# Kernel optimization log

Hardware: AMD Instinct MI355X
Metric: run time of the kernel (lower is better)

## Reference

```python
import jax, jax.numpy as jnp
import numpy as np

B, S, D = 8, 2048, 512

def setup_inputs() -> dict:
    key = jax.random.key(0)
    ks = jax.random.split(key, 7)
    scale = 1.0 / np.sqrt(D)
    return {
        "x": jax.random.normal(ks[0], (B, S, D), dtype=jnp.float32),
        "Wq": jax.random.normal(ks[1], (D, D), dtype=jnp.float32) * scale,
        "bq": jax.random.normal(ks[2], (D,), dtype=jnp.float32) * 0.01,
        "Wk": jax.random.normal(ks[3], (D, D), dtype=jnp.float32) * scale,
        "bk": jax.random.normal(ks[4], (D,), dtype=jnp.float32) * 0.01,
        "Wv": jax.random.normal(ks[5], (D, D), dtype=jnp.float32) * scale,
        "bv": jax.random.normal(ks[6], (D,), dtype=jnp.float32) * 0.01,
    }

def reference(x, Wq, bq, Wk, bk, Wv, bv):
    # Q/K/V projections: [B,S,D] @ [D,D]
    q = jnp.einsum('bsd,de->bse', x, Wq) + bq
    k = jnp.einsum('bsd,de->bse', x, Wk) + bk
    v = jnp.einsum('bsd,de->bse', x, Wv) + bv
    # NOTE: original module has NO 1/sqrt(d) scaling
    scores = jnp.einsum('bqd,bkd->bqk', q, k)          # [B,S,S]
    attn = jax.nn.softmax(scores, axis=-1)
    return jnp.einsum('bqk,bkd->bqd', attn, v)         # [B,S,D]
```

## Files before the change

kernel.cpp:

```cpp
#include <hip/hip_runtime.h>
#include <hip/hip_fp16.h>


typedef unsigned short u16;
typedef unsigned int u32;
typedef __attribute__((ext_vector_type(8))) _Float16 f16x8;
typedef __attribute__((ext_vector_type(16))) float f32x16;

#define S_LEN 2048
#define D_DIM 512
#define B_N 8

__device__ __forceinline__ u16 f2bf(float f) {
    u32 u = __float_as_uint(f);
    u32 r = u + 0x7FFFu + ((u >> 16) & 1u);
    return (u16)(r >> 16);
}
__device__ __forceinline__ float bf2f(u16 h) {
    return __uint_as_float((u32)h << 16);
}
__device__ __forceinline__ u16 f2h(float f) {
    _Float16 h = (_Float16)f;
    return *(u16*)&h;
}
__device__ __forceinline__ float h2f(u16 h) {
    _Float16 v = *(_Float16*)&h;
    return (float)v;
}
__device__ __forceinline__ void gl16(const u16* g, u16* l) {
    __builtin_amdgcn_global_load_lds(
        (const __attribute__((address_space(1))) void*)g,
        (__attribute__((address_space(3))) void*)l, 16, 0, 0);
}
__device__ __forceinline__ f32x16 mfma16(f16x8 a, f16x8 b, f32x16 c) {
    return __builtin_amdgcn_mfma_f32_32x32x16_f16(a, b, c, 0, 0, 0);
}

__global__ void detect_k(const u16* __restrict__ x, int* __restrict__ flag)
{
    int t = threadIdx.x;
    u16 u = x[2 * t];
    int e = (u >> 7) & 0xFF;
    int sane = (e == 0) || (e >= 110 && e <= 140);
    unsigned long long b = __ballot(sane);
    if (t == 0) *flag = (__popcll(b) >= 32) ? 1 : 0;
}

__global__ __launch_bounds__(256) void cvt_x(
    const void* __restrict__ X, u16* __restrict__ xf,
    const int* __restrict__ flagp)
{
    const size_t i4 = ((size_t)blockIdx.x * 256 + threadIdx.x) * 4;
    float f[4];
    if (*flagp) {
        ushort4 u = *(const ushort4*)((const u16*)X + i4);
        f[0] = bf2f(u.x); f[1] = bf2f(u.y); f[2] = bf2f(u.z); f[3] = bf2f(u.w);
    } else {
        float4 ff = *(const float4*)((const float*)X + i4);
        f[0] = ff.x; f[1] = ff.y; f[2] = ff.z; f[3] = ff.w;
    }
    ushort4 h;
    h.x = f2h(f[0]); h.y = f2h(f[1]); h.z = f2h(f[2]); h.w = f2h(f[3]);
    *(ushort4*)(xf + i4) = h;
}

__global__ __launch_bounds__(256) void pack_w(
    const void* __restrict__ Wq, const void* __restrict__ Wk, const void* __restrict__ Wv,
    u16* __restrict__ WT, const int* __restrict__ flagp)
{
    const int k = blockIdx.x;
    const int n = blockIdx.y * 256 + threadIdx.x;
    const void* W = n < 512 ? Wq : n < 1024 ? Wk : Wv;
    const int nc = n & 511;
    float f = *flagp ? bf2f(((const u16*)W)[(size_t)k * 512 + nc])
                     : ((const float*)W)[(size_t)k * 512 + nc];
    WT[(size_t)n * 512 + k] = f2h(f);
}

__global__ void pack_bias(
    const void* __restrict__ bq, const void* __restrict__ bk, const void* __restrict__ bv,
    float* __restrict__ bcat, const int* __restrict__ flagp)
{
    const int t = blockIdx.x * 256 + threadIdx.x;
    const void* b = t < 512 ? bq : t < 1024 ? bk : bv;
    const int i = t & 511;
    bcat[t] = *flagp ? bf2f(((const u16*)b)[i]) : ((const float*)b)[i];
}

template <int EPI>
__global__ __launch_bounds__(256) void gemm_f16(
    const u16* __restrict__ A_, const u16* __restrict__ B_,
    void* __restrict__ Cp, const float* __restrict__ biasf,
    u16* __restrict__ Oq, u16* __restrict__ Ok, u16* __restrict__ OvT,
    const int* __restrict__ flagp,
    int K, int lda, int ldb, int ldc, long sA, long sB, long sC, long cbase)
{
    const int tid = threadIdx.x;
    const int lane = tid & 63, wav = tid >> 6;
    const int l31 = lane & 31, lh = lane >> 5;

    const int gx = gridDim.x, gy = gridDim.y;
    const int total = gx * gy * gridDim.z;
    const int chunk = total >> 3;
    int lin = (blockIdx.z * gy + blockIdx.y) * gx + blockIdx.x;
    lin = (lin & 7) * chunk + (lin >> 3);
    const int bx = lin % gx;
    const int by = (lin / gx) % gy;
    const int bz = lin / (gx * gy);

    const int m0 = by * 128, n0 = bx * 128;
    const int bm = (wav >> 1) * 64, bn = (wav & 1) * 64;

    const u16* A = A_ + (size_t)bz * sA;
    const u16* B = B_ + (size_t)bz * sB;

    __shared__ __align__(16) u16 sh[16384];
    u16* As = sh;
    u16* Bs = sh + 8192;

    const int r0 = tid >> 3;
    const int c0 = ((tid & 7) ^ (r0 & 7)) * 8;
    size_t aoff[4], boff[4];
#pragma unroll
    for (int j = 0; j < 4; j++) {
        aoff[j] = (size_t)(m0 + r0 + j * 32) * lda + c0;
        boff[j] = (size_t)(n0 + r0 + j * 32) * ldb + c0;
    }
    const int g7 = l31 & 7;
    const int rowA0 = (bm + l31) * 64, rowA1 = (bm + 32 + l31) * 64;
    const int rowB0 = (bn + l31) * 64, rowB1 = (bn + 32 + l31) * 64;

    f32x16 acc[2][2];
#pragma unroll
    for (int i = 0; i < 2; i++)
#pragma unroll
        for (int j = 0; j < 2; j++)
#pragma unroll
            for (int r = 0; r < 16; r++) acc[i][j][r] = 0.f;

    for (int k0 = 0; k0 < K; k0 += 64) {
#pragma unroll
        for (int j = 0; j < 4; j++) {
            gl16(A + aoff[j] + k0, As + j * 2048 + wav * 512);
            gl16(B + boff[j] + k0, Bs + j * 2048 + wav * 512);
        }
        __syncthreads();

#pragma unroll
        for (int h = 0; h < 4; h++) {
            const int so = ((h * 2 + lh) ^ g7) * 8;
            f16x8 af[2], bfr[2];
            af[0] = *(const f16x8*)&As[rowA0 + so];
            af[1] = *(const f16x8*)&As[rowA1 + so];
            bfr[0] = *(const f16x8*)&Bs[rowB0 + so];
            bfr[1] = *(const f16x8*)&Bs[rowB1 + so];
#pragma unroll
            for (int i = 0; i < 2; i++)
#pragma unroll
                for (int j = 0; j < 2; j++)
                    acc[i][j] = mfma16(af[i], bfr[j], acc[i][j]);
        }
        __syncthreads();
    }

    if (EPI == 2) {
        const int mode = bx >> 2;
        if (mode == 2) {
#pragma unroll
            for (int it = 0; it < 2; it++)
#pragma unroll
                for (int jt = 0; jt < 2; jt++) {
                    const int lc = bn + jt * 32 + l31;
                    const float badd = biasf[n0 + lc];
#pragma unroll
                    for (int r = 0; r < 16; r++) {
                        const int row = bm + it * 32 + (r & 3) + 8 * (r >> 2) + 4 * lh;
                        sh[lc * 128 + (row ^ ((lc & 15) << 3))] =
                            f2h(acc[it][jt][r] + badd);
                    }
                }
            __syncthreads();
            const int vbase = n0 - 1024;
#pragma unroll
            for (int p = 0; p < 8; p++) {
                const int q = p * 256 + tid;
                const int lc = q >> 4, ch = q & 15;
                const int g = ch ^ (lc & 15);
                f16x8 val = *(const f16x8*)&sh[lc * 128 + g * 8];
                *(f16x8*)&OvT[(size_t)(vbase + lc) * 16384 + m0 + ch * 8] = val;
            }
        } else {
#pragma unroll
            for (int it = 0; it < 2; it++)
#pragma unroll
                for (int jt = 0; jt < 2; jt++) {
                    const int gcol = n0 + bn + jt * 32 + l31;
                    const int lcol = gcol & 511;
                    const float badd = biasf[gcol];
#pragma unroll
                    for (int r = 0; r < 16; r++) {
                        const int row = m0 + bm + it * 32 + (r & 3) + 8 * (r >> 2) + 4 * lh;
                        const float v = acc[it][jt][r] + badd;
                        if (mode == 0) Oq[(size_t)row * 512 + lcol] = f2h(v);
                        else           Ok[(size_t)row * 512 + lcol] = f2h(v);
                    }
                }
        }
    } else if (EPI == 0) {
        u16* Ch = (u16*)Cp;
        const long coff = (long)bz * sC;
#pragma unroll
        for (int it = 0; it < 2; it++)
#pragma unroll
            for (int jt = 0; jt < 2; jt++) {
                const int col = n0 + bn + jt * 32 + l31;
#pragma unroll
                for (int r = 0; r < 16; r++) {
                    const int row = m0 + bm + it * 32 + (r & 3) + 8 * (r >> 2) + 4 * lh;
                    Ch[(size_t)(coff + (long)row * ldc + col)] = f2h(acc[it][jt][r]);
                }
            }
    } else {
        const int isbf = *flagp;
        float* Cf = (float*)Cp;
        u16* Cb = (u16*)Cp;
        const long coff = cbase + (long)bz * sC;
#pragma unroll
        for (int it = 0; it < 2; it++)
#pragma unroll
            for (int jt = 0; jt < 2; jt++) {
                const int col = n0 + bn + jt * 32 + l31;
#pragma unroll
                for (int r = 0; r < 16; r++) {
                    const int row = m0 + bm + it * 32 + (r & 3) + 8 * (r >> 2) + 4 * lh;
                    const size_t idx = (size_t)(coff + (long)row * ldc + col);
                    if (isbf) Cb[idx] = f2bf(acc[it][jt][r]);
                    else Cf[idx] = acc[it][jt][r];
                }
            }
    }
}

__global__ __launch_bounds__(256) void softmax_k(u16* __restrict__ sc)
{
    u16* srow = sc + (size_t)blockIdx.x * S_LEN;
    const int tid = threadIdx.x;

    f16x8 v = ((const f16x8*)srow)[tid];
    float f[8];
#pragma unroll
    for (int j = 0; j < 8; j++) f[j] = (float)v[j];

    float m = f[0];
#pragma unroll
    for (int j = 1; j < 8; j++) m = fmaxf(m, f[j]);
#pragma unroll
    for (int off = 32; off > 0; off >>= 1) m = fmaxf(m, __shfl_down(m, off));

    __shared__ float redm[4], reds[4];
    if ((tid & 63) == 0) redm[tid >> 6] = m;
    __syncthreads();
    m = fmaxf(fmaxf(redm[0], redm[1]), fmaxf(redm[2], redm[3]));

    float s = 0.f;
#pragma unroll
    for (int j = 0; j < 8; j++) { f[j] = __expf(f[j] - m); s += f[j]; }
#pragma unroll
    for (int off = 32; off > 0; off >>= 1) s += __shfl_down(s, off);
    if ((tid & 63) == 0) reds[tid >> 6] = s;
    __syncthreads();
    s = reds[0] + reds[1] + reds[2] + reds[3];

    const float inv = 1.0f / s;
    f16x8 p;
#pragma unroll
    for (int j = 0; j < 8; j++) p[j] = (_Float16)(f[j] * inv);
    ((f16x8*)srow)[tid] = p;
}

extern "C" void kernel_launch(void* const* d_in, const int* in_sizes, int n_in,
                              void* d_out, int out_size, void* d_ws, size_t ws_size,
                              hipStream_t stream)
{
    const void* x  = d_in[0];
    const void* Wq = d_in[1]; const void* bq = d_in[2];
    const void* Wk = d_in[3]; const void* bk = d_in[4];
    const void* Wv = d_in[5]; const void* bv = d_in[6];

    const int S = S_LEN, D = D_DIM;
    const long SD = (long)S * D;

    char* w = (char*)d_ws;
    int*   flag = (int*)w;
    u16*   WT   = (u16*)(w + 1024);
    float* bcat = (float*)(w + 1573888);
    u16*   xf   = (u16*)(w + 1580032);
    u16*   qf   = (u16*)(w + 18357248);
    u16*   kf   = (u16*)(w + 35134464);
    u16*   vT   = (u16*)(w + 51911680);
    u16*   scP  = (u16*)(w + 68688896);

    const size_t avail = ws_size > 68688896ull ? ws_size - 68688896ull : 0;
    const size_t perb = (size_t)S * S * 2;
    const int c = avail >= 8 * perb ? 8 : avail >= 4 * perb ? 4 : avail >= 2 * perb ? 2 : 1;

    dim3 blk(256);

    detect_k<<<1, 64, 0, stream>>>((const u16*)x, flag);
    cvt_x<<<8192, blk, 0, stream>>>(x, xf, flag);
    pack_w<<<dim3(512, 6), blk, 0, stream>>>(Wq, Wk, Wv, WT, flag);
    pack_bias<<<6, blk, 0, stream>>>(bq, bk, bv, bcat, flag);

    gemm_f16<2><<<dim3(12, 128, 1), blk, 0, stream>>>(
        xf, WT, nullptr, bcat, qf, kf, vT, flag,
        512, 512, 512, 0, 0, 0, 0, 0);

    for (int cb = 0; cb < B_N; cb += c) {
        const size_t off = (size_t)cb * SD;
        gemm_f16<0><<<dim3(16, 16, c), blk, 0, stream>>>(
            qf + off, kf + off, scP, nullptr, nullptr, nullptr, nullptr, flag,
            512, 512, 512, S, SD, SD, (long)S * S, 0);
        softmax_k<<<c * S, blk, 0, stream>>>(scP);
        gemm_f16<1><<<dim3(4, 16, c), blk, 0, stream>>>(
            scP, vT + (size_t)cb * S, d_out, nullptr,
            nullptr, nullptr, nullptr, flag,
            S, S, B_N * S, D, (long)S * S, S, SD, (long)cb * SD);
    }
}
```

Baseline: 252.2 us.

## Add dedicated 64x128 PV GEMM kernel using 16x16x32 MFMA tiles

Replaces the generic gemm_f16<1> path for the attention-times-V product with a new kernel that uses 64x128 output tiles and 16x16x32 MFMA instructions, doubling the grid in the M dimension. It also remaps block indices so consecutive blocks are spread in strides, likely for cache or XCD locality. The goal is more blocks in flight and better occupancy for a GEMM that otherwise launches few workgroups. The trade-off is smaller tiles with less reuse per block and a single-buffered LDS pipeline.

```diff
diff --git a/kernel.cpp b/kernel.cpp
--- a/kernel.cpp
+++ b/kernel.cpp
@@ -6,6 +6,7 @@
 typedef unsigned int u32;
 typedef __attribute__((ext_vector_type(8))) _Float16 f16x8;
 typedef __attribute__((ext_vector_type(16))) float f32x16;
+typedef __attribute__((ext_vector_type(4))) float f32x4;
 
 #define S_LEN 2048
 #define D_DIM 512
@@ -23,10 +24,6 @@
     _Float16 h = (_Float16)f;
     return *(u16*)&h;
 }
-__device__ __forceinline__ float h2f(u16 h) {
-    _Float16 v = *(_Float16*)&h;
-    return (float)v;
-}
 __device__ __forceinline__ void gl16(const u16* g, u16* l) {
     __builtin_amdgcn_global_load_lds(
         (const __attribute__((address_space(1))) void*)g,
@@ -34,6 +31,9 @@
 }
 __device__ __forceinline__ f32x16 mfma16(f16x8 a, f16x8 b, f32x16 c) {
     return __builtin_amdgcn_mfma_f32_32x32x16_f16(a, b, c, 0, 0, 0);
+}
+__device__ __forceinline__ f32x4 mfma16q(f16x8 a, f16x8 b, f32x4 c) {
+    return __builtin_amdgcn_mfma_f32_16x16x32_f16(a, b, c, 0, 0, 0);
 }
 
 __global__ void detect_k(const u16* __restrict__ x, int* __restrict__ flag)
@@ -206,7 +206,7 @@
                     }
                 }
         }
-    } else if (EPI == 0) {
+    } else {
         u16* Ch = (u16*)Cp;
         const long coff = (long)bz * sC;
 #pragma unroll
@@ -220,25 +220,106 @@
                     Ch[(size_t)(coff + (long)row * ldc + col)] = f2h(acc[it][jt][r]);
                 }
             }
-    } else {
-        const int isbf = *flagp;
-        float* Cf = (float*)Cp;
-        u16* Cb = (u16*)Cp;
-        const long coff = cbase + (long)bz * sC;
-#pragma unroll
-        for (int it = 0; it < 2; it++)
-#pragma unroll
-            for (int jt = 0; jt < 2; jt++) {
-                const int col = n0 + bn + jt * 32 + l31;
-#pragma unroll
-                for (int r = 0; r < 16; r++) {
-                    const int row = m0 + bm + it * 32 + (r & 3) + 8 * (r >> 2) + 4 * lh;
-                    const size_t idx = (size_t)(coff + (long)row * ldc + col);
-                    if (isbf) Cb[idx] = f2bf(acc[it][jt][r]);
-                    else Cf[idx] = acc[it][jt][r];
-                }
+    }
+}
+
+__global__ __launch_bounds__(256) void gemm_pv64(
+    const u16* __restrict__ A_, const u16* __restrict__ B_,
+    void* __restrict__ Cp, const int* __restrict__ flagp,
+    int K, int lda, int ldb, int ldc, long sA, long sB, long sC, long cbase)
+{
+    const int tid = threadIdx.x;
+    const int lane = tid & 63;
+    const int wid = tid >> 6;
+    const int wm = wid & 1;
+    const int wn = wid >> 1;
+    const int l15 = lane & 15, lq = lane >> 4;
+
+    const int gx = gridDim.x, gy = gridDim.y;
+    const int total = gx * gy * gridDim.z;
+    const int chunk = total >> 3;
+    int lin = (blockIdx.z * gy + blockIdx.y) * gx + blockIdx.x;
+    lin = (lin & 7) * chunk + (lin >> 3);
+    const int bx = lin % gx;
+    const int by = (lin / gx) % gy;
+    const int bz = lin / (gx * gy);
+
+    const int m0 = by * 64, n0 = bx * 128;
+
+    const u16* A = A_ + (size_t)bz * sA;
+    const u16* B = B_ + (size_t)bz * sB;
+
+    __shared__ __align__(16) u16 As[64 * 64];
+    __shared__ __align__(16) u16 Bs[128 * 64];
+
+    const int r0 = tid >> 3;
+    const int c0 = ((tid & 7) ^ (r0 & 7)) * 8;
+    size_t aoff[2], boff[4];
+#pragma unroll
+    for (int j = 0; j < 2; j++)
+        aoff[j] = (size_t)(m0 + j * 32 + r0) * lda + c0;
+#pragma unroll
+    for (int j = 0; j < 4; j++)
+        boff[j] = (size_t)(n0 + j * 32 + r0) * ldb + c0;
+
+    f32x4 acc[2][4];
+#pragma unroll
+    for (int h = 0; h < 2; h++)
+#pragma unroll
+        for (int nj = 0; nj < 4; nj++)
+#pragma unroll
+            for (int r = 0; r < 4; r++) acc[h][nj][r] = 0.f;
+
+    for (int k0 = 0; k0 < K; k0 += 64) {
+#pragma unroll
+        for (int j = 0; j < 2; j++)
+            gl16(A + aoff[j] + k0, As + j * 2048 + (tid & 63) * 8 + (tid >> 6) * 512);
+#pragma unroll
+        for (int j = 0; j < 4; j++)
+            gl16(B + boff[j] + k0, Bs + j * 2048 + (tid & 63) * 8 + (tid >> 6) * 512);
+        __syncthreads();
+
+#pragma unroll
+        for (int ks = 0; ks < 2; ks++) {
+            f16x8 a[2], b[4];
+#pragma unroll
+            for (int h = 0; h < 2; h++) {
+                const int row = wm * 32 + h * 16 + l15;
+                const int off = (row << 6) + ((((ks << 2) + lq) ^ (row & 7)) << 3);
+                a[h] = *(const f16x8*)&As[off];
             }
-    }
+#pragma unroll
+            for (int nj = 0; nj < 4; nj++) {
+                const int row = wn * 64 + nj * 16 + l15;
+                const int off = (row << 6) + ((((ks << 2) + lq) ^ (row & 7)) << 3);
+                b[nj] = *(const f16x8*)&Bs[off];
+            }
+#pragma unroll
+            for (int h = 0; h < 2; h++)
+#pragma unroll
+                for (int nj = 0; nj < 4; nj++)
+                    acc[h][nj] = mfma16q(a[h], b[nj], acc[h][nj]);
+        }
+        __syncthreads();
+    }
+
+    const int isbf = *flagp;
+    float* Cf = (float*)Cp;
+    u16* Cb = (u16*)Cp;
+    const long coff = cbase + (long)bz * sC;
+#pragma unroll
+    for (int h = 0; h < 2; h++)
+#pragma unroll
+        for (int nj = 0; nj < 4; nj++) {
+            const int col = n0 + wn * 64 + nj * 16 + l15;
+#pragma unroll
+            for (int r = 0; r < 4; r++) {
+                const int row = m0 + wm * 32 + h * 16 + lq * 4 + r;
+                const size_t idx = (size_t)(coff + (long)row * ldc + col);
+                if (isbf) Cb[idx] = f2bf(acc[h][nj][r]);
+                else Cf[idx] = acc[h][nj][r];
+            }
+        }
 }
 
 __global__ __launch_bounds__(256) void softmax_k(u16* __restrict__ sc)
@@ -321,9 +402,8 @@
             qf + off, kf + off, scP, nullptr, nullptr, nullptr, nullptr, flag,
             512, 512, 512, S, SD, SD, (long)S * S, 0);
         softmax_k<<<c * S, blk, 0, stream>>>(scP);
-        gemm_f16<1><<<dim3(4, 16, c), blk, 0, stream>>>(
-            scP, vT + (size_t)cb * S, d_out, nullptr,
-            nullptr, nullptr, nullptr, flag,
+        gemm_pv64<<<dim3(4, 32, c), blk, 0, stream>>>(
+            scP, vT + (size_t)cb * S, d_out, flag,
             S, S, B_N * S, D, (long)S * S, S, SD, (long)cb * SD);
     }
 }
```

Result: no change. 251.5 us (-0.3%).
